# Kernel tuning notes

Hardware: AMD Instinct MI355X
Metric: run time of the kernel (lower is better)

Reference implementation:

```python
import jax, jax.numpy as jnp
import numpy as np
import math

B, N, F = 32, 1024, 64      # batch, nodes, input_dim (data_size)
PRE = 64                     # preweight (== input_dim so output Linear works)
L1 = 128                     # layer_1


def setup_inputs() -> dict:
    key = jax.random.key(0)
    ks = jax.random.split(key, 12)
    def lin(k, out_d, in_d):
        bound = 1.0 / math.sqrt(in_d)
        kw, kb = jax.random.split(k)
        W = jax.random.uniform(kw, (out_d, in_d), jnp.float32, -bound, bound)
        b = jax.random.uniform(kb, (out_d,), jnp.float32, -bound, bound)
        return W, b
    W_pre, b_pre = lin(ks[0], PRE, F)
    W_fc1, b_fc1 = lin(ks[1], L1, PRE)
    W_keys, b_keys = lin(ks[2], 1, L1)
    W_out, b_out = lin(ks[3], 1, F)
    alpha = jax.random.uniform(ks[4], (1,), jnp.float32)
    x = jax.random.normal(ks[5], (B, N, F), jnp.float32)
    adjacency_matrix = jax.random.uniform(ks[6], (B, N, N), jnp.float32)
    return {
        "x": x, "adjacency_matrix": adjacency_matrix, "alpha": alpha,
        "W_pre": W_pre, "b_pre": b_pre, "W_fc1": W_fc1, "b_fc1": b_fc1,
        "W_keys": W_keys, "b_keys": b_keys, "W_out": W_out, "b_out": b_out,
    }


def reference(x, adjacency_matrix, alpha, W_pre, b_pre, W_fc1, b_fc1,
              W_keys, b_keys, W_out, b_out):
    # --- D^-1/2 A D^-1/2 normalization (D is diagonal -> row/col scaling) ---
    deg = adjacency_matrix.sum(axis=-1)                       # [B, N]
    deg = jnp.where(deg != 0, deg, 1.0)
    d_isqrt = deg ** -0.5                                     # [B, N]
    A_norm = d_isqrt[:, :, None] * adjacency_matrix * d_isqrt[:, None, :]
    # --- (alpha*I + A_norm) @ x ---
    h = alpha[0] * x + jnp.einsum('bij,bjf->bif', A_norm, x)  # [B, N, F]
    # --- node embedding (pre_weighting + relu) ---
    values = jax.nn.relu(h @ W_pre.T + b_pre)                 # [B, N, PRE]
    # --- attention pooling (dropout is identity at eval) ---
    queries = jax.nn.relu(values @ W_fc1.T + b_fc1)           # [B, N, L1]
    logits = (queries @ W_keys.T + b_keys)[..., 0]            # [B, N]
    scores = jax.nn.softmax(logits / math.sqrt(2.0), axis=-1) # [B, N]
    vect = jnp.einsum('bn,bnp->bp', scores, values)           # [B, PRE]
    y = vect @ W_out.T + b_out                                # [B, 1]
    return y
```

## Files before the change

### kernel.cpp

```cpp
#include <hip/hip_runtime.h>


#define N_ 1024
#define F_ 64

typedef short s16x8 __attribute__((ext_vector_type(8)));
typedef float f32x4 __attribute__((ext_vector_type(4)));
typedef unsigned short u16x4 __attribute__((ext_vector_type(4)));
typedef unsigned short u16x8 __attribute__((ext_vector_type(8)));

__device__ __forceinline__ unsigned short bf16rne(float f) {
  union { float f; unsigned u; } v; v.f = f;
  unsigned r = v.u + 0x7fffu + ((v.u >> 16) & 1u);
  return (unsigned short)(r >> 16);
}

__device__ __forceinline__ void fma_row(float (&a)[4], const float4 av,
                                        const float4 x0, const float4 x1,
                                        const float4 x2, const float4 x3) {
  a[0] += av.x * x0.x + av.y * x1.x + av.z * x2.x + av.w * x3.x;
  a[1] += av.x * x0.y + av.y * x1.y + av.z * x2.y + av.w * x3.y;
  a[2] += av.x * x0.z + av.y * x1.z + av.z * x2.z + av.w * x3.z;
  a[3] += av.x * x0.w + av.y * x1.w + av.z * x2.w + av.w * x3.w;
}

__device__ __forceinline__ void stage16(const unsigned short* g, void* l) {
  auto gp = reinterpret_cast<const __attribute__((address_space(1))) void*>(
      reinterpret_cast<uintptr_t>(g));
  auto lp = reinterpret_cast<__attribute__((address_space(3))) void*>(
      reinterpret_cast<uintptr_t>(l));
  __builtin_amdgcn_global_load_lds(gp, lp, 16, 0, 0);
}

__global__ __launch_bounds__(256) void k_prep(const float* __restrict__ A,
                                              float* __restrict__ disq,
                                              unsigned short* __restrict__ Abf) {
  const int row  = blockIdx.x * 4 + (threadIdx.x >> 6);
  const int lane = threadIdx.x & 63;
  const float4* a4 = (const float4*)(A + (size_t)row * N_);
  unsigned short* ob = Abf + (size_t)row * N_;
  float s = 0.f;
#pragma unroll
  for (int it = 0; it < 4; ++it) {
    float4 v = a4[it * 64 + lane];
    s += v.x + v.y + v.z + v.w;
    u16x4 o;
    o[0] = bf16rne(v.x); o[1] = bf16rne(v.y);
    o[2] = bf16rne(v.z); o[3] = bf16rne(v.w);
    *(u16x4*)(ob + (it * 64 + lane) * 4) = o;
  }
#pragma unroll
  for (int off = 32; off > 0; off >>= 1) s += __shfl_down(s, off, 64);
  if (lane == 0) {
    float d = (s != 0.f) ? s : 1.f;
    disq[row] = rsqrtf(d);
  }
}

__global__ __launch_bounds__(256) void k_xt(const float* __restrict__ x,
                                            const float* __restrict__ disq,
                                            unsigned short* __restrict__ xtb) {
  __shared__ float xs[64][68];
  const int b = blockIdx.y, j0 = blockIdx.x * 64, t = threadIdx.x;
  const float* xb = x + ((size_t)b << 16);
  const float* dq = disq + (b << 10);
#pragma unroll
  for (int it = 0; it < 4; ++it) {
    int idx = it * 1024 + t * 4;
    int jj = idx >> 6, ff = idx & 63;
    float4 vv = *(const float4*)&xb[(size_t)(j0 + jj) * F_ + ff];
    float sc = dq[j0 + jj];
    vv.x *= sc; vv.y *= sc; vv.z *= sc; vv.w *= sc;
    *(float4*)&xs[jj][ff] = vv;
  }
  __syncthreads();
  const int f = t & 63, ch = t >> 6;
  u16x8 o0, o1;
#pragma unroll
  for (int jj = 0; jj < 8; ++jj) o0[jj] = bf16rne(xs[ch * 16 + jj][f]);
#pragma unroll
  for (int jj = 0; jj < 8; ++jj) o1[jj] = bf16rne(xs[ch * 16 + 8 + jj][f]);
  unsigned short* dst = xtb + (size_t)(b * 64 + f) * N_ + j0 + ch * 16;
  *(u16x8*)dst = o0;
  *(u16x8*)(dst + 8) = o1;
}

__global__ __launch_bounds__(256, 3) void k_spmm_mlp(const unsigned short* __restrict__ Abf,
                                                     const unsigned short* __restrict__ xtb,
                                                     const float* __restrict__ x,
                                                     const float* __restrict__ disq,
                                                     const float* __restrict__ alphap,
                                                     const float* __restrict__ Wpre,
                                                     const float* __restrict__ bpre,
                                                     const float* __restrict__ Wfc1,
                                                     const float* __restrict__ bfc1,
                                                     const float* __restrict__ Wkeys,
                                                     const float* __restrict__ bkeysp,
                                                     float* __restrict__ values,
                                                     float* __restrict__ logits) {
  __shared__ __attribute__((aligned(16))) char smem[54272];
  float (*hs)[68]   = (float(*)[68])(smem);
  float (*wft)[128] = (float(*)[128])(smem + 17408);
  float (*part)[16] = (float(*)[16])(smem + 50176);

  const int t  = threadIdx.x;
  const int b  = blockIdx.x;
  const int i0 = blockIdx.y * 64;
  const int w  = t >> 6, l = t & 63;
  const int lr = l & 15, kq = l >> 4;

  const int srow = l >> 3;
  const int sch  = ((l & 7) ^ srow) * 8;
  const int half = (w & 1) * 32;
  const unsigned short* gsA = Abf + ((size_t)b << 20) + (size_t)(i0 + half + srow) * N_ + sch;
  const unsigned short* gsB = xtb + (size_t)(b * 64 + half + srow) * N_ + sch;
  const int loff = half * 128;

  auto STAGE = [&](char* bufp, int ksv) {
    const int ko = ksv * 64;
    if (w < 2) {
#pragma unroll
      for (int j = 0; j < 4; ++j)
        stage16(gsA + (size_t)j * 8 * N_ + ko, bufp + loff + j * 1024);
    } else {
#pragma unroll
      for (int j = 0; j < 4; ++j)
        stage16(gsB + (size_t)j * 8 * N_ + ko, bufp + 8192 + loff + j * 1024);
    }
  };

  STAGE(smem, 0);
  __syncthreads();

  f32x4 acc0 = {0.f, 0.f, 0.f, 0.f}, acc1 = acc0, acc2 = acc0, acc3 = acc0;
  const int arow = w * 16 + lr;
  const int sw = (lr & 7) << 4;
  int cur = 0;

  for (int ks = 0; ks < 16; ++ks) {
    if (ks < 15) STAGE(smem + (cur ^ 1) * 16384, ks + 1);
    const char* cb = smem + cur * 16384;
#pragma unroll
    for (int s = 0; s < 2; ++s) {
      const int ch = ((kq + 4 * s) << 4);
      s16x8 af = *(const s16x8*)(cb + arow * 128 + (ch ^ sw));
      s16x8 b0 = *(const s16x8*)(cb + 8192 + (0 * 16 + lr) * 128 + (ch ^ sw));
      s16x8 b1 = *(const s16x8*)(cb + 8192 + (1 * 16 + lr) * 128 + (ch ^ sw));
      s16x8 b2 = *(const s16x8*)(cb + 8192 + (2 * 16 + lr) * 128 + (ch ^ sw));
      s16x8 b3 = *(const s16x8*)(cb + 8192 + (3 * 16 + lr) * 128 + (ch ^ sw));
      acc0 = __builtin_amdgcn_mfma_f32_16x16x32_bf16(af, b0, acc0, 0, 0, 0);
      acc1 = __builtin_amdgcn_mfma_f32_16x16x32_bf16(af, b1, acc1, 0, 0, 0);
      acc2 = __builtin_amdgcn_mfma_f32_16x16x32_bf16(af, b2, acc2, 0, 0, 0);
      acc3 = __builtin_amdgcn_mfma_f32_16x16x32_bf16(af, b3, acc3, 0, 0, 0);
    }
    __syncthreads();
    cur ^= 1;
  }

  const float alpha = alphap[0];
  const float* dq = disq + (b << 10);
  const float* xb = x + ((size_t)b << 16);
  const int rl = w * 16 + kq * 4;
#pragma unroll
  for (int r = 0; r < 4; ++r) {
    float di = dq[i0 + rl + r];
    size_t ro = (size_t)(i0 + rl + r) * F_;
    hs[rl + r][0  + lr] = alpha * xb[ro + 0  + lr] + di * acc0[r];
    hs[rl + r][16 + lr] = alpha * xb[ro + 16 + lr] + di * acc1[r];
    hs[rl + r][32 + lr] = alpha * xb[ro + 32 + lr] + di * acc2[r];
    hs[rl + r][48 + lr] = alpha * xb[ro + 48 + lr] + di * acc3[r];
  }
#pragma unroll
  for (int it = 0; it < 4; ++it) {
    int idx = it * 1024 + t * 4;
    float4 wv = *(const float4*)&Wpre[idx];
    int p = idx >> 6, f = idx & 63;
    wft[f + 0][p] = wv.x; wft[f + 1][p] = wv.y; wft[f + 2][p] = wv.z; wft[f + 3][p] = wv.w;
  }
  __syncthreads();

  const size_t base = ((size_t)(b * 16 + blockIdx.y)) * 4096;
  const int cg = t & 15, rg = t >> 4;
  float acc[4][4] = {{0.f}};
#pragma unroll
  for (int q = 0; q < 16; ++q) {
    float4 xv0 = *(float4*)&wft[q * 4 + 0][cg * 4];
    float4 xv1 = *(float4*)&wft[q * 4 + 1][cg * 4];
    float4 xv2 = *(float4*)&wft[q * 4 + 2][cg * 4];
    float4 xv3 = *(float4*)&wft[q * 4 + 3][cg * 4];
#pragma unroll
    for (int k = 0; k < 4; ++k) {
      float4 av = *(float4*)&hs[rg * 4 + k][q * 4];
      fma_row(acc[k], av, xv0, xv1, xv2, xv3);
    }
  }
  float4 bp = *(const float4*)&bpre[cg * 4];
  __syncthreads();
#pragma unroll
  for (int k = 0; k < 4; ++k) {
    float4 o;
    o.x = fmaxf(acc[k][0] + bp.x, 0.f);
    o.y = fmaxf(acc[k][1] + bp.y, 0.f);
    o.z = fmaxf(acc[k][2] + bp.z, 0.f);
    o.w = fmaxf(acc[k][3] + bp.w, 0.f);
    *(float4*)&hs[rg * 4 + k][cg * 4] = o;
    *(float4*)&values[base + (size_t)(rg * 4 + k) * 64 + cg * 4] = o;
  }
#pragma unroll
  for (int it = 0; it < 8; ++it) {
    int idx = it * 1024 + t * 4;
    int ll = idx >> 6, p = idx & 63;
    float4 wv = *(const float4*)&Wfc1[idx];
    wft[p + 0][ll] = wv.x; wft[p + 1][ll] = wv.y; wft[p + 2][ll] = wv.z; wft[p + 3][ll] = wv.w;
  }
  __syncthreads();

  const int lg = cg;
  float acc_a[4][4] = {{0.f}};
  float acc_b[4][4] = {{0.f}};
#pragma unroll
  for (int q = 0; q < 16; ++q) {
    float4 w0a = *(float4*)&wft[q * 4 + 0][lg * 8];
    float4 w0b = *(float4*)&wft[q * 4 + 0][lg * 8 + 4];
    float4 w1a = *(float4*)&wft[q * 4 + 1][lg * 8];
    float4 w1b = *(float4*)&wft[q * 4 + 1][lg * 8 + 4];
    float4 w2a = *(float4*)&wft[q * 4 + 2][lg * 8];
    float4 w2b = *(float4*)&wft[q * 4 + 2][lg * 8 + 4];
    float4 w3a = *(float4*)&wft[q * 4 + 3][lg * 8];
    float4 w3b = *(float4*)&wft[q * 4 + 3][lg * 8 + 4];
#pragma unroll
    for (int k = 0; k < 4; ++k) {
      float4 vv = *(float4*)&hs[rg * 4 + k][q * 4];
      fma_row(acc_a[k], vv, w0a, w1a, w2a, w3a);
      fma_row(acc_b[k], vv, w0b, w1b, w2b, w3b);
    }
  }
  float4 bfa = *(const float4*)&bfc1[lg * 8];
  float4 bfb = *(const float4*)&bfc1[lg * 8 + 4];
  float4 wka = *(const float4*)&Wkeys[lg * 8];
  float4 wkb = *(const float4*)&Wkeys[lg * 8 + 4];
#pragma unroll
  for (int k = 0; k < 4; ++k) {
    float lp = 0.f;
    lp += fmaxf(acc_a[k][0] + bfa.x, 0.f) * wka.x;
    lp += fmaxf(acc_a[k][1] + bfa.y, 0.f) * wka.y;
    lp += fmaxf(acc_a[k][2] + bfa.z, 0.f) * wka.z;
    lp += fmaxf(acc_a[k][3] + bfa.w, 0.f) * wka.w;
    lp += fmaxf(acc_b[k][0] + bfb.x, 0.f) * wkb.x;
    lp += fmaxf(acc_b[k][1] + bfb.y, 0.f) * wkb.y;
    lp += fmaxf(acc_b[k][2] + bfb.z, 0.f) * wkb.z;
    lp += fmaxf(acc_b[k][3] + bfb.w, 0.f) * wkb.w;
    part[rg * 4 + k][lg] = lp;
  }
  __syncthreads();
  if (t < 64) {
    float s = bkeysp[0];
#pragma unroll
    for (int g = 0; g < 16; ++g) s += part[t][g];
    logits[(b * 16 + blockIdx.y) * 64 + t] = s;
  }
}

__global__ __launch_bounds__(1024) void k_tail(const float* __restrict__ logits,
                                               const float* __restrict__ values,
                                               float* __restrict__ vpart) {
  const int c = blockIdx.x, b = blockIdx.y, t = threadIdx.x;
  __shared__ float sc[1024];
  __shared__ float red[16];
  __shared__ float pool[16][64];
  const float isq2 = 0.70710678118654752f;
  float lv = logits[(b << 10) + t] * isq2;
  float m = lv;
#pragma unroll
  for (int off = 32; off > 0; off >>= 1) m = fmaxf(m, __shfl_xor(m, off, 64));
  if ((t & 63) == 0) red[t >> 6] = m;
  __syncthreads();
  m = red[0];
#pragma unroll
  for (int i = 1; i < 16; ++i) m = fmaxf(m, red[i]);
  float e = expf(lv - m);
  float s = e;
#pragma unroll
  for (int off = 32; off > 0; off >>= 1) s += __shfl_xor(s, off, 64);
  __syncthreads();
  if ((t & 63) == 0) red[t >> 6] = s;
  __syncthreads();
  s = red[0];
#pragma unroll
  for (int i = 1; i < 16; ++i) s += red[i];
  sc[t] = e * (1.f / s);
  __syncthreads();
  const int col = t & 63, g = t >> 6;
  const float* vb = values + ((size_t)b << 16);
  float acc = 0.f;
#pragma unroll
  for (int k = 0; k < 8; ++k) {
    int n = c * 128 + g + 16 * k;
    acc += sc[n] * vb[(size_t)n * 64 + col];
  }
  pool[g][col] = acc;
  __syncthreads();
  if (t < 64) {
    float v = 0.f;
#pragma unroll
    for (int gg = 0; gg < 16; ++gg) v += pool[gg][t];
    vpart[(b * 8 + c) * 64 + t] = v;
  }
}

__global__ __launch_bounds__(256) void k_out(const float* __restrict__ vpart,
                                             const float* __restrict__ Wout,
                                             const float* __restrict__ boutp,
                                             float* __restrict__ y) {
  const int t = threadIdx.x, w = t >> 6, lane = t & 63;
#pragma unroll
  for (int it = 0; it < 8; ++it) {
    int b = w * 8 + it;
    float v = 0.f;
#pragma unroll
    for (int ch = 0; ch < 8; ++ch) v += vpart[(b * 8 + ch) * 64 + lane];
    float p = v * Wout[lane];
#pragma unroll
    for (int off = 32; off > 0; off >>= 1) p += __shfl_down(p, off, 64);
    if (lane == 0) y[b] = p + boutp[0];
  }
}

extern "C" void kernel_launch(void* const* d_in, const int* in_sizes, int n_in,
                              void* d_out, int out_size, void* d_ws, size_t ws_size,
                              hipStream_t stream) {
  const float* x     = (const float*)d_in[0];
  const float* A     = (const float*)d_in[1];
  const float* alpha = (const float*)d_in[2];
  const float* Wpre  = (const float*)d_in[3];
  const float* bpre  = (const float*)d_in[4];
  const float* Wfc1  = (const float*)d_in[5];
  const float* bfc1  = (const float*)d_in[6];
  const float* Wkeys = (const float*)d_in[7];
  const float* bkeys = (const float*)d_in[8];
  const float* Wout  = (const float*)d_in[9];
  const float* bout  = (const float*)d_in[10];
  float* y = (float*)d_out;

  float* ws     = (float*)d_ws;
  float* disq   = ws;
  float* values = disq + 32768;
  float* logits = values + 2097152;
  float* vpart  = logits + 32768;
  unsigned short* xtb = (unsigned short*)(vpart + 16384);
  unsigned short* Abf = xtb + 2097152;

  k_prep    <<<dim3(8192),   dim3(256),  0, stream>>>(A, disq, Abf);
  k_xt      <<<dim3(16, 32), dim3(256),  0, stream>>>(x, disq, xtb);
  k_spmm_mlp<<<dim3(32, 16), dim3(256),  0, stream>>>(Abf, xtb, x, disq, alpha,
                                                      Wpre, bpre, Wfc1, bfc1, Wkeys, bkeys,
                                                      values, logits);
  k_tail    <<<dim3(8, 32),  dim3(1024), 0, stream>>>(logits, values, vpart);
  k_out     <<<dim3(1),      dim3(256),  0, stream>>>(vpart, Wout, bout, y);
}
```

Baseline: 78.06 us.

## Fuse bf16 conversion of adjacency into SpMM by staging fp32 A directly

The prep kernel no longer writes a bf16 copy of the adjacency matrix; it now only computes the degree normalization. The SpMM kernel stages fp32 A tiles into LDS with a new swizzled layout and converts them to bf16 in registers just before the MFMA. This removes a large intermediate write and its read-back. In exchange, the main kernel reads twice as many bytes of A, uses a larger LDS double buffer, and does extra conversion ALU work in the inner loop.

After: 76.88 us (median of 2 runs). No clear change (-1.5%).

```diff
diff --git a/kernel.cpp b/kernel.cpp
--- a/kernel.cpp
+++ b/kernel.cpp
@@ -6,7 +6,6 @@
 
 typedef short s16x8 __attribute__((ext_vector_type(8)));
 typedef float f32x4 __attribute__((ext_vector_type(4)));
-typedef unsigned short u16x4 __attribute__((ext_vector_type(4)));
 typedef unsigned short u16x8 __attribute__((ext_vector_type(8)));
 
 __device__ __forceinline__ unsigned short bf16rne(float f) {
@@ -24,7 +23,7 @@
   a[3] += av.x * x0.w + av.y * x1.w + av.z * x2.w + av.w * x3.w;
 }
 
-__device__ __forceinline__ void stage16(const unsigned short* g, void* l) {
+__device__ __forceinline__ void stage16(const void* g, void* l) {
   auto gp = reinterpret_cast<const __attribute__((address_space(1))) void*>(
       reinterpret_cast<uintptr_t>(g));
   auto lp = reinterpret_cast<__attribute__((address_space(3))) void*>(
@@ -32,22 +31,16 @@
   __builtin_amdgcn_global_load_lds(gp, lp, 16, 0, 0);
 }
 
-__global__ __launch_bounds__(256) void k_prep(const float* __restrict__ A,
-                                              float* __restrict__ disq,
-                                              unsigned short* __restrict__ Abf) {
+__global__ __launch_bounds__(256) void k_deg(const float* __restrict__ A,
+                                             float* __restrict__ disq) {
   const int row  = blockIdx.x * 4 + (threadIdx.x >> 6);
   const int lane = threadIdx.x & 63;
   const float4* a4 = (const float4*)(A + (size_t)row * N_);
-  unsigned short* ob = Abf + (size_t)row * N_;
   float s = 0.f;
 #pragma unroll
   for (int it = 0; it < 4; ++it) {
     float4 v = a4[it * 64 + lane];
     s += v.x + v.y + v.z + v.w;
-    u16x4 o;
-    o[0] = bf16rne(v.x); o[1] = bf16rne(v.y);
-    o[2] = bf16rne(v.z); o[3] = bf16rne(v.w);
-    *(u16x4*)(ob + (it * 64 + lane) * 4) = o;
   }
 #pragma unroll
   for (int off = 32; off > 0; off >>= 1) s += __shfl_down(s, off, 64);
@@ -85,7 +78,7 @@
   *(u16x8*)(dst + 8) = o1;
 }
 
-__global__ __launch_bounds__(256, 3) void k_spmm_mlp(const unsigned short* __restrict__ Abf,
+__global__ __launch_bounds__(256, 3) void k_spmm_mlp(const float* __restrict__ Af,
                                                      const unsigned short* __restrict__ xtb,
                                                      const float* __restrict__ x,
                                                      const float* __restrict__ disq,
@@ -108,24 +101,32 @@
   const int i0 = blockIdx.y * 64;
   const int w  = t >> 6, l = t & 63;
   const int lr = l & 15, kq = l >> 4;
-
-  const int srow = l >> 3;
-  const int sch  = ((l & 7) ^ srow) * 8;
+  const size_t bb = ((size_t)b << 20);
+
   const int half = (w & 1) * 32;
-  const unsigned short* gsA = Abf + ((size_t)b << 20) + (size_t)(i0 + half + srow) * N_ + sch;
-  const unsigned short* gsB = xtb + (size_t)(b * 64 + half + srow) * N_ + sch;
-  const int loff = half * 128;
+  const int srow4 = l >> 4;
+  const int mslot = l & 15;
+  const float* gA0 = Af + bb + (size_t)(i0 + half + srow4) * 1024;
+  int xoff[4];
+#pragma unroll
+  for (int q = 0; q < 4; ++q) xoff[q] = (mslot ^ ((q * 4 + srow4) & 15)) << 2;
+  const int srow8 = l >> 3;
+  const int schB  = ((l & 7) ^ srow8) * 8;
+  const unsigned short* gsB = xtb + (size_t)(b * 64 + half + srow8) * N_ + schB;
 
   auto STAGE = [&](char* bufp, int ksv) {
-    const int ko = ksv * 64;
     if (w < 2) {
+      const int ko = ksv * 64;
+#pragma unroll
+      for (int j = 0; j < 8; ++j)
+        stage16(gA0 + (size_t)j * 4096 + xoff[j & 3] + ko,
+                bufp + (half + j * 4) * 256);
+    } else {
+      const int ko = ksv * 64;
 #pragma unroll
       for (int j = 0; j < 4; ++j)
-        stage16(gsA + (size_t)j * 8 * N_ + ko, bufp + loff + j * 1024);
-    } else {
-#pragma unroll
-      for (int j = 0; j < 4; ++j)
-        stage16(gsB + (size_t)j * 8 * N_ + ko, bufp + 8192 + loff + j * 1024);
+        stage16(gsB + (size_t)j * 8 * N_ + ko,
+                bufp + 16384 + half * 128 + j * 1024);
     }
   };
 
@@ -134,20 +135,27 @@
 
   f32x4 acc0 = {0.f, 0.f, 0.f, 0.f}, acc1 = acc0, acc2 = acc0, acc3 = acc0;
   const int arow = w * 16 + lr;
-  const int sw = (lr & 7) << 4;
+  const int swB = (lr & 7) << 4;
   int cur = 0;
 
   for (int ks = 0; ks < 16; ++ks) {
-    if (ks < 15) STAGE(smem + (cur ^ 1) * 16384, ks + 1);
-    const char* cb = smem + cur * 16384;
+    if (ks < 15) STAGE(smem + (cur ^ 1) * 24576, ks + 1);
+    const char* cb = smem + cur * 24576;
 #pragma unroll
     for (int s = 0; s < 2; ++s) {
+      const int m0 = s * 8 + kq * 2;
+      f32x4 alo = *(const f32x4*)(cb + arow * 256 + ((m0 ^ lr) << 4));
+      f32x4 ahi = *(const f32x4*)(cb + arow * 256 + (((m0 + 1) ^ lr) << 4));
+      s16x8 af;
+      af[0] = (short)bf16rne(alo[0]); af[1] = (short)bf16rne(alo[1]);
+      af[2] = (short)bf16rne(alo[2]); af[3] = (short)bf16rne(alo[3]);
+      af[4] = (short)bf16rne(ahi[0]); af[5] = (short)bf16rne(ahi[1]);
+      af[6] = (short)bf16rne(ahi[2]); af[7] = (short)bf16rne(ahi[3]);
       const int ch = ((kq + 4 * s) << 4);
-      s16x8 af = *(const s16x8*)(cb + arow * 128 + (ch ^ sw));
-      s16x8 b0 = *(const s16x8*)(cb + 8192 + (0 * 16 + lr) * 128 + (ch ^ sw));
-      s16x8 b1 = *(const s16x8*)(cb + 8192 + (1 * 16 + lr) * 128 + (ch ^ sw));
-      s16x8 b2 = *(const s16x8*)(cb + 8192 + (2 * 16 + lr) * 128 + (ch ^ sw));
-      s16x8 b3 = *(const s16x8*)(cb + 8192 + (3 * 16 + lr) * 128 + (ch ^ sw));
+      s16x8 b0 = *(const s16x8*)(cb + 16384 + (0 * 16 + lr) * 128 + (ch ^ swB));
+      s16x8 b1 = *(const s16x8*)(cb + 16384 + (1 * 16 + lr) * 128 + (ch ^ swB));
+      s16x8 b2 = *(const s16x8*)(cb + 16384 + (2 * 16 + lr) * 128 + (ch ^ swB));
+      s16x8 b3 = *(const s16x8*)(cb + 16384 + (3 * 16 + lr) * 128 + (ch ^ swB));
       acc0 = __builtin_amdgcn_mfma_f32_16x16x32_bf16(af, b0, acc0, 0, 0, 0);
       acc1 = __builtin_amdgcn_mfma_f32_16x16x32_bf16(af, b1, acc1, 0, 0, 0);
       acc2 = __builtin_amdgcn_mfma_f32_16x16x32_bf16(af, b2, acc2, 0, 0, 0);
@@ -348,11 +356,10 @@
   float* logits = values + 2097152;
   float* vpart  = logits + 32768;
   unsigned short* xtb = (unsigned short*)(vpart + 16384);
-  unsigned short* Abf = xtb + 2097152;
-
-  k_prep    <<<dim3(8192),   dim3(256),  0, stream>>>(A, disq, Abf);
+
+  k_deg     <<<dim3(8192),   dim3(256),  0, stream>>>(A, disq);
   k_xt      <<<dim3(16, 32), dim3(256),  0, stream>>>(x, disq, xtb);
-  k_spmm_mlp<<<dim3(32, 16), dim3(256),  0, stream>>>(Abf, xtb, x, disq, alpha,
+  k_spmm_mlp<<<dim3(32, 16), dim3(256),  0, stream>>>(A, xtb, x, disq, alpha,
                                                       Wpre, bpre, Wfc1, bfc1, Wkeys, bkeys,
                                                       values, logits);
   k_tail    <<<dim3(8, 32),  dim3(1024), 0, stream>>>(logits, values, vpart);
```

## Pre-pack A and x into MFMA fragment layout and drop LDS staging

Applied to the files above, without the earlier changes.

The prep kernels now write the bf16 adjacency and scaled-transposed x directly in per-lane MFMA fragment order, so each wave in the SpMM kernel loads its A/B operands straight from global memory with contiguous 16-byte loads. The LDS double-buffered global_load_lds pipeline and its per-step barriers are removed. k_prep2 processes 8 rows per block through LDS to build the packed tiles, and launch bounds occupancy drops from 3 to 2. The trade-off is that B fragments are reread from global/L2 by every wave with no LDS sharing, relying on cache hits and unrolled loads for latency hiding.

Result: slower. 87.19 us (+11.7%).

```diff
diff --git a/kernel.cpp b/kernel.cpp
--- a/kernel.cpp
+++ b/kernel.cpp
@@ -6,7 +6,6 @@
 
 typedef short s16x8 __attribute__((ext_vector_type(8)));
 typedef float f32x4 __attribute__((ext_vector_type(4)));
-typedef unsigned short u16x4 __attribute__((ext_vector_type(4)));
 typedef unsigned short u16x8 __attribute__((ext_vector_type(8)));
 
 __device__ __forceinline__ unsigned short bf16rne(float f) {
@@ -24,42 +23,57 @@
   a[3] += av.x * x0.w + av.y * x1.w + av.z * x2.w + av.w * x3.w;
 }
 
-__device__ __forceinline__ void stage16(const unsigned short* g, void* l) {
-  auto gp = reinterpret_cast<const __attribute__((address_space(1))) void*>(
-      reinterpret_cast<uintptr_t>(g));
-  auto lp = reinterpret_cast<__attribute__((address_space(3))) void*>(
-      reinterpret_cast<uintptr_t>(l));
-  __builtin_amdgcn_global_load_lds(gp, lp, 16, 0, 0);
-}
-
-__global__ __launch_bounds__(256) void k_prep(const float* __restrict__ A,
-                                              float* __restrict__ disq,
-                                              unsigned short* __restrict__ Abf) {
-  const int row  = blockIdx.x * 4 + (threadIdx.x >> 6);
-  const int lane = threadIdx.x & 63;
-  const float4* a4 = (const float4*)(A + (size_t)row * N_);
-  unsigned short* ob = Abf + (size_t)row * N_;
-  float s = 0.f;
-#pragma unroll
-  for (int it = 0; it < 4; ++it) {
-    float4 v = a4[it * 64 + lane];
-    s += v.x + v.y + v.z + v.w;
-    u16x4 o;
-    o[0] = bf16rne(v.x); o[1] = bf16rne(v.y);
-    o[2] = bf16rne(v.z); o[3] = bf16rne(v.w);
-    *(u16x4*)(ob + (it * 64 + lane) * 4) = o;
-  }
-#pragma unroll
-  for (int off = 32; off > 0; off >>= 1) s += __shfl_down(s, off, 64);
-  if (lane == 0) {
-    float d = (s != 0.f) ? s : 1.f;
-    disq[row] = rsqrtf(d);
+__global__ __launch_bounds__(256) void k_prep2(const float* __restrict__ A,
+                                               float* __restrict__ disq,
+                                               unsigned short* __restrict__ Abf_p) {
+  __shared__ float As[8][1032];
+  __shared__ float red[8][4];
+  const int blk = blockIdx.x, t = threadIdx.x;
+  const float* Ab = A + (size_t)blk * 8192;
+  float psum[8];
+#pragma unroll
+  for (int it = 0; it < 8; ++it) {
+    float4 v = *(const float4*)&Ab[it * 1024 + t * 4];
+    *(float4*)&As[it][t * 4] = v;
+    psum[it] = v.x + v.y + v.z + v.w;
+  }
+  const int w = t >> 6, lane = t & 63;
+#pragma unroll
+  for (int it = 0; it < 8; ++it) {
+    float s = psum[it];
+#pragma unroll
+    for (int off = 32; off > 0; off >>= 1) s += __shfl_down(s, off, 64);
+    if (lane == 0) red[it][w] = s;
+  }
+  __syncthreads();
+  if (t < 8) {
+    float d = red[t][0] + red[t][1] + red[t][2] + red[t][3];
+    d = (d != 0.f) ? d : 1.f;
+    disq[blk * 8 + t] = rsqrtf(d);
+  }
+  const int b = blk >> 7;
+  const int itile = (blk & 127) >> 1;
+  const int rb8 = (blk & 1) * 8;
+  unsigned short* base = Abf_p + (((size_t)(b * 64 + itile)) * 32) * 512;
+#pragma unroll
+  for (int rep = 0; rep < 4; ++rep) {
+    int c = rep * 256 + t;
+    int kt = c >> 5, q = (c >> 3) & 3, r8 = c & 7;
+    const float* src = &As[r8][kt * 32 + q * 8];
+    f32x4 lo = *(const f32x4*)src;
+    f32x4 hi = *(const f32x4*)(src + 4);
+    u16x8 o;
+    o[0] = bf16rne(lo[0]); o[1] = bf16rne(lo[1]);
+    o[2] = bf16rne(lo[2]); o[3] = bf16rne(lo[3]);
+    o[4] = bf16rne(hi[0]); o[5] = bf16rne(hi[1]);
+    o[6] = bf16rne(hi[2]); o[7] = bf16rne(hi[3]);
+    *(u16x8*)(base + kt * 512 + (q * 16 + rb8 + r8) * 8) = o;
   }
 }
 
 __global__ __launch_bounds__(256) void k_xt(const float* __restrict__ x,
                                             const float* __restrict__ disq,
-                                            unsigned short* __restrict__ xtb) {
+                                            unsigned short* __restrict__ xtb_p) {
   __shared__ float xs[64][68];
   const int b = blockIdx.y, j0 = blockIdx.x * 64, t = threadIdx.x;
   const float* xb = x + ((size_t)b << 16);
@@ -74,19 +88,24 @@
     *(float4*)&xs[jj][ff] = vv;
   }
   __syncthreads();
-  const int f = t & 63, ch = t >> 6;
-  u16x8 o0, o1;
-#pragma unroll
-  for (int jj = 0; jj < 8; ++jj) o0[jj] = bf16rne(xs[ch * 16 + jj][f]);
-#pragma unroll
-  for (int jj = 0; jj < 8; ++jj) o1[jj] = bf16rne(xs[ch * 16 + 8 + jj][f]);
-  unsigned short* dst = xtb + (size_t)(b * 64 + f) * N_ + j0 + ch * 16;
-  *(u16x8*)dst = o0;
-  *(u16x8*)(dst + 8) = o1;
-}
-
-__global__ __launch_bounds__(256, 3) void k_spmm_mlp(const unsigned short* __restrict__ Abf,
-                                                     const unsigned short* __restrict__ xtb,
+#pragma unroll
+  for (int rep = 0; rep < 2; ++rep) {
+    int ch = rep * 256 + t;
+    int tile = ch >> 6;
+    int l = ch & 63, q = l >> 4, r = l & 15;
+    int kt2 = tile >> 2, c = tile & 3;
+    int jl = kt2 * 32 + q * 8;
+    int col = c * 16 + r;
+    u16x8 o;
+#pragma unroll
+    for (int jj = 0; jj < 8; ++jj) o[jj] = bf16rne(xs[jl + jj][col]);
+    int ktg = blockIdx.x * 2 + kt2;
+    *(u16x8*)(xtb_p + (((size_t)(b * 4 + c)) * 32 + ktg) * 512 + l * 8) = o;
+  }
+}
+
+__global__ __launch_bounds__(256, 2) void k_spmm_mlp(const unsigned short* __restrict__ Abf_p,
+                                                     const unsigned short* __restrict__ xtb_p,
                                                      const float* __restrict__ x,
                                                      const float* __restrict__ disq,
                                                      const float* __restrict__ alphap,
@@ -109,52 +128,21 @@
   const int w  = t >> 6, l = t & 63;
   const int lr = l & 15, kq = l >> 4;
 
-  const int srow = l >> 3;
-  const int sch  = ((l & 7) ^ srow) * 8;
-  const int half = (w & 1) * 32;
-  const unsigned short* gsA = Abf + ((size_t)b << 20) + (size_t)(i0 + half + srow) * N_ + sch;
-  const unsigned short* gsB = xtb + (size_t)(b * 64 + half + srow) * N_ + sch;
-  const int loff = half * 128;
-
-  auto STAGE = [&](char* bufp, int ksv) {
-    const int ko = ksv * 64;
-    if (w < 2) {
-#pragma unroll
-      for (int j = 0; j < 4; ++j)
-        stage16(gsA + (size_t)j * 8 * N_ + ko, bufp + loff + j * 1024);
-    } else {
-#pragma unroll
-      for (int j = 0; j < 4; ++j)
-        stage16(gsB + (size_t)j * 8 * N_ + ko, bufp + 8192 + loff + j * 1024);
-    }
-  };
-
-  STAGE(smem, 0);
-  __syncthreads();
+  const unsigned short* Ap = Abf_p + (((size_t)(b * 64 + blockIdx.y * 4 + w)) * 32) * 512 + l * 8;
+  const unsigned short* Bp = xtb_p + (((size_t)(b * 4)) * 32) * 512 + l * 8;
 
   f32x4 acc0 = {0.f, 0.f, 0.f, 0.f}, acc1 = acc0, acc2 = acc0, acc3 = acc0;
-  const int arow = w * 16 + lr;
-  const int sw = (lr & 7) << 4;
-  int cur = 0;
-
-  for (int ks = 0; ks < 16; ++ks) {
-    if (ks < 15) STAGE(smem + (cur ^ 1) * 16384, ks + 1);
-    const char* cb = smem + cur * 16384;
-#pragma unroll
-    for (int s = 0; s < 2; ++s) {
-      const int ch = ((kq + 4 * s) << 4);
-      s16x8 af = *(const s16x8*)(cb + arow * 128 + (ch ^ sw));
-      s16x8 b0 = *(const s16x8*)(cb + 8192 + (0 * 16 + lr) * 128 + (ch ^ sw));
-      s16x8 b1 = *(const s16x8*)(cb + 8192 + (1 * 16 + lr) * 128 + (ch ^ sw));
-      s16x8 b2 = *(const s16x8*)(cb + 8192 + (2 * 16 + lr) * 128 + (ch ^ sw));
-      s16x8 b3 = *(const s16x8*)(cb + 8192 + (3 * 16 + lr) * 128 + (ch ^ sw));
-      acc0 = __builtin_amdgcn_mfma_f32_16x16x32_bf16(af, b0, acc0, 0, 0, 0);
-      acc1 = __builtin_amdgcn_mfma_f32_16x16x32_bf16(af, b1, acc1, 0, 0, 0);
-      acc2 = __builtin_amdgcn_mfma_f32_16x16x32_bf16(af, b2, acc2, 0, 0, 0);
-      acc3 = __builtin_amdgcn_mfma_f32_16x16x32_bf16(af, b3, acc3, 0, 0, 0);
-    }
-    __syncthreads();
-    cur ^= 1;
+#pragma unroll 8
+  for (int kt = 0; kt < 32; ++kt) {
+    s16x8 af = *(const s16x8*)(Ap + kt * 512);
+    s16x8 b0 = *(const s16x8*)(Bp + kt * 512);
+    s16x8 b1 = *(const s16x8*)(Bp + 16384 + kt * 512);
+    s16x8 b2 = *(const s16x8*)(Bp + 32768 + kt * 512);
+    s16x8 b3 = *(const s16x8*)(Bp + 49152 + kt * 512);
+    acc0 = __builtin_amdgcn_mfma_f32_16x16x32_bf16(af, b0, acc0, 0, 0, 0);
+    acc1 = __builtin_amdgcn_mfma_f32_16x16x32_bf16(af, b1, acc1, 0, 0, 0);
+    acc2 = __builtin_amdgcn_mfma_f32_16x16x32_bf16(af, b2, acc2, 0, 0, 0);
+    acc3 = __builtin_amdgcn_mfma_f32_16x16x32_bf16(af, b3, acc3, 0, 0, 0);
   }
 
   const float alpha = alphap[0];
@@ -347,12 +335,12 @@
   float* values = disq + 32768;
   float* logits = values + 2097152;
   float* vpart  = logits + 32768;
-  unsigned short* xtb = (unsigned short*)(vpart + 16384);
-  unsigned short* Abf = xtb + 2097152;
-
-  k_prep    <<<dim3(8192),   dim3(256),  0, stream>>>(A, disq, Abf);
-  k_xt      <<<dim3(16, 32), dim3(256),  0, stream>>>(x, disq, xtb);
-  k_spmm_mlp<<<dim3(32, 16), dim3(256),  0, stream>>>(Abf, xtb, x, disq, alpha,
+  unsigned short* xtb_p = (unsigned short*)(vpart + 16384);
+  unsigned short* Abf_p = xtb_p + 2097152;
+
+  k_prep2   <<<dim3(4096),   dim3(256),  0, stream>>>(A, disq, Abf_p);
+  k_xt      <<<dim3(16, 32), dim3(256),  0, stream>>>(x, disq, xtb_p);
+  k_spmm_mlp<<<dim3(32, 16), dim3(256),  0, stream>>>(Abf_p, xtb_p, x, disq, alpha,
                                                       Wpre, bpre, Wfc1, bfc1, Wkeys, bkeys,
                                                       values, logits);
   k_tail    <<<dim3(8, 32),  dim3(1024), 0, stream>>>(logits, values, vpart);
```
